# Optimization experiments

Hardware: AMD Instinct MI355X
Metric: run time of the kernel (lower is better)

## Reference

```python
import jax, jax.numpy as jnp
import numpy as np
import math

B, S, D, H = 16, 1024, 1024, 16
HD = D // H                      # 64 head dim
MLP_H = int(int(D * 4.0) * 2 / 3)  # 2730 SwiGLU hidden
EPS = 1e-6


def _rmsnorm(h, w):
    # fp32 RMSNorm over last dim
    v = jnp.mean(h * h, axis=-1, keepdims=True)
    return w * (h * jax.lax.rsqrt(v + EPS))


def _rope(x):
    # x: [B, H, S, HD]; standard rotary, half-split convention
    hd = x.shape[-1]
    pos = jnp.arange(x.shape[-2], dtype=jnp.float32)
    inv = 1.0 / (10000.0 ** (jnp.arange(0, hd, 2, dtype=jnp.float32) / hd))
    fr = pos[:, None] * inv[None, :]          # [S, HD/2]
    cos, sin = jnp.cos(fr), jnp.sin(fr)
    x1, x2 = jnp.split(x, 2, axis=-1)
    return jnp.concatenate([x1 * cos - x2 * sin, x1 * sin + x2 * cos], axis=-1)


def setup_inputs() -> dict:
    key = jax.random.key(0)
    ks = jax.random.split(key, 16)
    sc = 0.02
    return {
        "x": jax.random.normal(ks[0], (B, S, D), jnp.float32),
        "c": jax.random.normal(ks[1], (B, D), jnp.float32),
        "w_qkv": jax.random.normal(ks[2], (D, 3 * D), jnp.float32) * sc,
        "b_qkv": jnp.zeros((3 * D,), jnp.float32),
        "w_proj": jax.random.normal(ks[3], (D, D), jnp.float32) * sc,
        "b_proj": jnp.zeros((D,), jnp.float32),
        "w12": jax.random.normal(ks[4], (D, 2 * MLP_H), jnp.float32) * sc,
        "b12": jnp.zeros((2 * MLP_H,), jnp.float32),
        "w3": jax.random.normal(ks[5], (MLP_H, D), jnp.float32) * sc,
        "b3": jnp.zeros((D,), jnp.float32),
        "w_ada": jax.random.normal(ks[6], (D, 6 * D), jnp.float32) * sc,
        "b_ada": jnp.zeros((6 * D,), jnp.float32),
        "norm1_w": jnp.ones((D,), jnp.float32),
        "norm2_w": jnp.ones((D,), jnp.float32),
        "qn_w": jnp.ones((HD,), jnp.float32),
        "kn_w": jnp.ones((HD,), jnp.float32),
    }


def _forward(x, c, w_qkv, b_qkv, w_proj, b_proj, w12, b12, w3, b3,
             w_ada, b_ada, norm1_w, norm2_w, qn_w, kn_w):
    # adaLN modulation params
    ada = jax.nn.silu(c) @ w_ada + b_ada               # [B, 6D]
    sh_a, sc_a, g_a, sh_m, sc_m, g_m = jnp.split(ada, 6, axis=-1)

    def modulate(h, shift, scale):
        return h * (1.0 + scale[:, None, :]) + shift[:, None, :]

    # --- attention branch ---
    h = modulate(_rmsnorm(x, norm1_w), sh_a, sc_a)     # [B, S, D]
    qkv = (h @ w_qkv + b_qkv).reshape(B, S, 3, H, HD)
    qkv = jnp.transpose(qkv, (2, 0, 3, 1, 4))          # [3, B, H, S, HD]
    q, k, v = qkv[0], qkv[1], qkv[2]
    q = _rope(_rmsnorm(q, qn_w))
    k = _rope(_rmsnorm(k, kn_w))
    scores = jnp.einsum('bhqd,bhkd->bhqk', q, k) / math.sqrt(HD)
    attn = jax.nn.softmax(scores, axis=-1)
    o = jnp.einsum('bhqk,bhkd->bhqd', attn, v)         # [B, H, S, HD]
    o = jnp.transpose(o, (0, 2, 1, 3)).reshape(B, S, D)
    o = o @ w_proj + b_proj
    x = x + g_a[:, None, :] * o

    # --- SwiGLU MLP branch ---
    h = modulate(_rmsnorm(x, norm2_w), sh_m, sc_m)
    x12 = h @ w12 + b12
    x1, x2 = jnp.split(x12, 2, axis=-1)
    mlp = (jax.nn.silu(x1) * x2) @ w3 + b3
    return x + g_m[:, None, :] * mlp


def reference(x, c, w_qkv, b_qkv, w_proj, b_proj, w12, b12, w3, b3,
              w_ada, b_ada, norm1_w, norm2_w, qn_w, kn_w):
    return _forward(x, c, w_qkv, b_qkv, w_proj, b_proj, w12, b12, w3, b3,
                    w_ada, b_ada, norm1_w, norm2_w, qn_w, kn_w)
```

## Files before the change

### kernel.cpp

```cpp
#include <hip/hip_runtime.h>
#include <hip/hip_bf16.h>
#include <math.h>

namespace {

constexpr int Bb = 16;
constexpr int Ss = 1024;
constexpr int Dd = 1024;
constexpr int Hh = 16;
constexpr int HD = 64;
constexpr int MLPH = 2730;
constexpr int MLPH_PAD = 2752;
constexpr int ADA_LD = 6144;
constexpr int NR = Bb * Ss;

typedef __attribute__((ext_vector_type(8))) short bf16x8;
typedef __attribute__((ext_vector_type(4))) float f32x4;
typedef __hip_bfloat16 bf16;
typedef unsigned int u32;

__device__ __forceinline__ float bf2f(bf16 v){ return __bfloat162float(v); }
__device__ __forceinline__ bf16 f2bf(float v){ return __float2bfloat16(v); }
__device__ __forceinline__ short f2bfs(float v){ bf16 t = __float2bfloat16(v); return __builtin_bit_cast(short, t); }

__device__ __forceinline__ f32x4 mfma16(bf16x8 a, bf16x8 b, f32x4 c){
  return __builtin_amdgcn_mfma_f32_16x16x32_bf16(a, b, c, 0, 0, 0);
}

__device__ __forceinline__ void gload16(const void* g, void* l){
  __builtin_amdgcn_global_load_lds(
      (const __attribute__((address_space(1))) u32*)g,
      (__attribute__((address_space(3))) u32*)l, 16, 0, 0);
}

__device__ __forceinline__ bf16x8 dsr128(const short* p){
  f32x4 r;
  asm volatile("ds_read_b128 %0, %1" : "=v"(r) : "v"((u32)(size_t)p));
  return __builtin_bit_cast(bf16x8, r);
}


__global__ void k_silu(const float* __restrict__ c, float* __restrict__ out, int n){
  int i = blockIdx.x*256 + threadIdx.x;
  if(i < n){ float v = c[i]; out[i] = v / (1.f + __expf(-v)); }
}

__global__ __launch_bounds__(256) void k_ada(const float* __restrict__ sc,
    const float* __restrict__ w, const float* __restrict__ bias, float* __restrict__ ada){
  __shared__ float red[4][Bb][64];
  int tid = threadIdx.x;
  int jj = tid & 63, ks = tid >> 6;
  int j = blockIdx.x*64 + jj;
  float acc[Bb];
  #pragma unroll
  for(int b=0;b<Bb;++b) acc[b] = 0.f;
  for(int k=ks*256; k<ks*256+256; ++k){
    float wv = w[(size_t)k*ADA_LD + j];
    #pragma unroll
    for(int b=0;b<Bb;++b) acc[b] += sc[b*Dd + k] * wv;
  }
  #pragma unroll
  for(int b=0;b<Bb;++b) red[ks][b][jj] = acc[b];
  __syncthreads();
  #pragma unroll
  for(int rep=0;rep<4;++rep){
    int idx = rep*256 + tid;
    int b = idx >> 6, j2 = idx & 63;
    float s = red[0][b][j2]+red[1][b][j2]+red[2][b][j2]+red[3][b][j2];
    ada[(size_t)b*ADA_LD + blockIdx.x*64 + j2] = s + bias[blockIdx.x*64 + j2];
  }
}

__global__ void k_rope_tab(float2* __restrict__ tab){
  int i = blockIdx.x*256 + threadIdx.x;
  int s = i >> 5, f = i & 31;
  float inv = powf(10000.f, -((float)(2*f)) / 64.f);
  float fr = (float)s * inv;
  float sv, cv;
  sincosf(fr, &sv, &cv);
  tab[i] = make_float2(cv, sv);
}

__global__ void k_transpose(const float* __restrict__ in, bf16* __restrict__ out,
                            int R, int C, int Rpad){
  __shared__ short tile[32][33];
  int tx = threadIdx.x & 31, ty = threadIdx.x >> 5;
  int tr0 = blockIdx.x*32, tc0 = blockIdx.y*32;
  #pragma unroll
  for(int i=0;i<4;++i){
    int r = tr0 + ty + i*8, cc = tc0 + tx;
    short v = 0;
    if(r < R && cc < C) v = f2bfs(in[(size_t)r*C + cc]);
    tile[ty+i*8][tx] = v;
  }
  __syncthreads();
  #pragma unroll
  for(int i=0;i<4;++i){
    int oc = tc0 + ty + i*8;
    int orow = tr0 + tx;
    if(oc < C && orow < Rpad)
      out[(size_t)oc*Rpad + orow] = __builtin_bit_cast(bf16, tile[tx][ty+i*8]);
  }
}

__global__ __launch_bounds__(256) void k_norm_mod(const float* __restrict__ x,
    const float* __restrict__ w, const float* __restrict__ shift, const float* __restrict__ scale,
    bf16* __restrict__ out){
  int r = blockIdx.x;
  int b = r >> 10;
  int t = threadIdx.x;
  const float* xr = x + (size_t)r*Dd;
  float v[4]; float ss = 0.f;
  #pragma unroll
  for(int i=0;i<4;++i){
    float f = xr[t*4+i];
    v[i] = f; ss += f*f;
  }
  #pragma unroll
  for(int m=1;m<64;m<<=1) ss += __shfl_xor(ss, m);
  __shared__ float red[4];
  if((t & 63) == 0) red[t>>6] = ss;
  __syncthreads();
  float tot = red[0]+red[1]+red[2]+red[3];
  float rms = rsqrtf(tot * (1.f/Dd) + 1e-6f);
  #pragma unroll
  for(int i=0;i<4;++i){
    int ccol = t*4+i;
    float h = v[i]*rms*w[ccol];
    float scv = scale[(size_t)b*ADA_LD + ccol];
    float shv = shift[(size_t)b*ADA_LD + ccol];
    out[(size_t)r*Dd + ccol] = f2bf(h*(1.f+scv) + shv);
  }
}

__global__ __launch_bounds__(256) void k_qknorm(bf16* __restrict__ qkv,
    const float* __restrict__ qw, const float* __restrict__ kw,
    const float2* __restrict__ tab){
  int bs = blockIdx.x;
  int s = bs & (Ss-1);
  int tid = threadIdx.x;
  int wv = tid >> 6, lane = tid & 63;
  int isK = wv >> 1;
  int chunk = (wv & 1)*64 + lane;
  int c = chunk & 7;
  int h = chunk >> 3;
  int dih = c*8;
  bf16* p = qkv + (size_t)bs*3072 + isK*Dd + h*HD + dih;
  bf16x8 v = *(const bf16x8*)p;
  float x[8]; float ss = 0.f;
  #pragma unroll
  for(int i=0;i<8;++i){ x[i] = bf2f(__builtin_bit_cast(bf16,(short)v[i])); ss += x[i]*x[i]; }
  ss += __shfl_xor(ss,1); ss += __shfl_xor(ss,2); ss += __shfl_xor(ss,4);
  float rms = rsqrtf(ss*(1.f/HD) + 1e-6f);
  const float* wn = isK ? kw : qw;
  float xn[8];
  #pragma unroll
  for(int i=0;i<8;++i) xn[i] = x[i]*rms*wn[dih+i];
  u32 pk[4], pq[4];
  #pragma unroll
  for(int i=0;i<4;++i)
    pk[i] = (u32)(unsigned short)f2bfs(xn[2*i]) |
            ((u32)(unsigned short)f2bfs(xn[2*i+1]) << 16);
  #pragma unroll
  for(int i=0;i<4;++i) pq[i] = __shfl_xor((int)pk[i], 4);
  float px[8];
  #pragma unroll
  for(int i=0;i<4;++i){
    px[2*i]   = bf2f(__builtin_bit_cast(bf16,(short)(pq[i] & 0xffff)));
    px[2*i+1] = bf2f(__builtin_bit_cast(bf16,(short)(pq[i] >> 16)));
  }
  const float2* tb = tab + s*32 + (c & 3)*8;
  float qs = isK ? 1.f : 0.18033688f;
  bf16x8 o;
  #pragma unroll
  for(int i=0;i<8;++i){
    float2 cs = tb[i];
    float r = (c < 4) ? (xn[i]*cs.x - px[i]*cs.y) : (px[i]*cs.y + xn[i]*cs.x);
    o[i] = f2bfs(r*qs);
  }
  *(bf16x8*)p = o;
}

#define LDA8(M,KH) dsr128(&Ah[((M)*16 + l15)*64 + ((((KH)*4 + l4) ^ l7))*8])
#define PHASE8(M0, STAGE_STMT, GATE_STMT) do{ \
  bf16x8 a0k0 = LDA8(M0,0), a0k1 = LDA8(M0,1), a1k0 = LDA8(M0+1,0), a1k1 = LDA8(M0+1,1); \
  STAGE_STMT; \
  __builtin_amdgcn_s_barrier(); \
  asm volatile("s_waitcnt lgkmcnt(0)" ::: "memory"); \
  __builtin_amdgcn_sched_barrier(0); \
  __builtin_amdgcn_s_setprio(1); \
  acc[M0][0]=mfma16(a0k0,bfrag[0][0],acc[M0][0]); \
  acc[M0][1]=mfma16(a0k0,bfrag[1][0],acc[M0][1]); \
  acc[M0][2]=mfma16(a0k0,bfrag[2][0],acc[M0][2]); \
  acc[M0][3]=mfma16(a0k0,bfrag[3][0],acc[M0][3]); \
  acc[M0+1][0]=mfma16(a1k0,bfrag[0][0],acc[M0+1][0]); \
  acc[M0+1][1]=mfma16(a1k0,bfrag[1][0],acc[M0+1][1]); \
  acc[M0+1][2]=mfma16(a1k0,bfrag[2][0],acc[M0+1][2]); \
  acc[M0+1][3]=mfma16(a1k0,bfrag[3][0],acc[M0+1][3]); \
  acc[M0][0]=mfma16(a0k1,bfrag[0][1],acc[M0][0]); \
  acc[M0][1]=mfma16(a0k1,bfrag[1][1],acc[M0][1]); \
  acc[M0][2]=mfma16(a0k1,bfrag[2][1],acc[M0][2]); \
  acc[M0][3]=mfma16(a0k1,bfrag[3][1],acc[M0][3]); \
  acc[M0+1][0]=mfma16(a1k1,bfrag[0][1],acc[M0+1][0]); \
  acc[M0+1][1]=mfma16(a1k1,bfrag[1][1],acc[M0+1][1]); \
  acc[M0+1][2]=mfma16(a1k1,bfrag[2][1],acc[M0+1][2]); \
  acc[M0+1][3]=mfma16(a1k1,bfrag[3][1],acc[M0+1][3]); \
  __builtin_amdgcn_s_setprio(0); \
  GATE_STMT; \
  __builtin_amdgcn_s_barrier(); }while(0)

template<int MODE>
__global__ __launch_bounds__(512, 2) void k_gemm8(
    const bf16* __restrict__ A, int lda,
    const bf16* __restrict__ BT, int ldb,
    const float* __restrict__ bias1, int K,
    const float* __restrict__ res, const float* __restrict__ gate,
    void* __restrict__ outp, int ldo)
{
  alignas(16) __shared__ short AH[2][2][128*64];
  alignas(16) __shared__ short BH[2][2][128*64];

  const int tid = threadIdx.x;
  const int lane = tid & 63, wid = tid >> 6;
  const int wm = wid >> 2, wn = wid & 3;
  const int l15 = lane & 15, l4 = lane >> 4;
  const int l7 = l15 & 7;
  const int brow = blockIdx.x * 256;
  const int bcol = blockIdx.y * 256;

  const int sr0 = tid >> 3;
  const int sr1 = sr0 + 64;
  const int sc  = ((tid & 7) ^ (sr0 & 7)) * 8;

  const bf16* Abase = A  + (size_t)brow*lda;
  const bf16* Bbase = BT + (size_t)bcol*ldb;

  auto stageA = [&](int t, int h){
    int d = t & 1;
    const bf16* g = Abase + (size_t)(h*128)*lda + t*64;
    gload16(g + (size_t)sr0*lda + sc, &AH[d][h][tid*8]);
    gload16(g + (size_t)sr1*lda + sc, &AH[d][h][(tid+512)*8]);
  };
  auto stageB = [&](int t, int h){
    int d = t & 1;
    const bf16* g = Bbase + (size_t)(h*128)*ldb + t*64;
    gload16(g + (size_t)sr0*ldb + sc, &BH[d][h][tid*8]);
    gload16(g + (size_t)sr1*ldb + sc, &BH[d][h][(tid+512)*8]);
  };

  f32x4 acc[8][4];
  f32x4 zero4 = {0.f,0.f,0.f,0.f};
  #pragma unroll
  for(int m=0;m<8;++m)
    #pragma unroll
    for(int n=0;n<4;++n) acc[m][n] = zero4;

  const int NT = K >> 6;
  stageA(0,0); stageA(0,1); stageB(0,0); stageB(0,1);
  stageB(1,0); stageB(1,1);
  asm volatile("s_waitcnt vmcnt(4)" ::: "memory");
  __builtin_amdgcn_sched_barrier(0);
  __builtin_amdgcn_s_barrier();

  const int bhsel = wn >> 1, brB = (wn & 1)*64;
  bf16x8 bfrag[4][2];

  for(int t=0; t<NT; ++t){
    const int d = t & 1;
    const short* Ah = AH[d][wm];
    const short* Bh = BH[d][bhsel];
    #pragma unroll
    for(int n=0;n<4;++n){
      int r = brB + n*16 + l15;
      bfrag[n][0] = dsr128(&Bh[r*64 + ((l4     ^ l7))*8]);
      bfrag[n][1] = dsr128(&Bh[r*64 + (((4|l4) ^ l7))*8]);
    }
    PHASE8(0, if(t+1 < NT) stageA(t+1,0), );
    PHASE8(2, if(t+1 < NT) stageA(t+1,1), );
    PHASE8(4, if(t+2 < NT) stageB(t+2,0), );
    PHASE8(6, if(t+2 < NT) stageB(t+2,1),
           asm volatile("s_waitcnt vmcnt(4)" ::: "memory");
           __builtin_amdgcn_sched_barrier(0) );
  }

  #pragma unroll
  for(int m=0;m<8;++m)
    #pragma unroll
    for(int n=0;n<4;++n)
      #pragma unroll
      for(int j=0;j<4;++j){
        int r  = brow + wm*128 + m*16 + l4*4 + j;
        int cc = bcol + wn*64  + n*16 + l15;
        float v = acc[m][n][j] + bias1[cc];
        if constexpr (MODE==0){
          ((bf16*)outp)[(size_t)r*ldo + cc] = f2bf(v);
        } else {
          int b = r >> 10;
          ((float*)outp)[(size_t)r*ldo + cc] =
              res[(size_t)r*Dd + cc] + gate[(size_t)b*ADA_LD + cc]*v;
        }
      }
}

__global__ __launch_bounds__(256, 2) void k_gemm3(
    const bf16* __restrict__ A, int lda,
    const bf16* __restrict__ BT, long long b2off, int ldb,
    const float* __restrict__ bias1, const float* __restrict__ bias2,
    int K, bf16* __restrict__ outp, int ldo)
{
  alignas(16) __shared__ short As[2][128*32];
  alignas(16) __shared__ short Bs[2][64*32];
  alignas(16) __shared__ short Bs2[2][64*32];

  int tid = threadIdx.x;
  int lane = tid & 63, wid = tid >> 6;
  int wm = wid >> 1, wn = wid & 1;
  int l15 = lane & 15, l4 = lane >> 4;
  int brow = blockIdx.x * 128;
  int bcol = blockIdx.y * 64;

  int r0 = tid >> 2, s0 = tid & 3;
  int r1 = r0 + 64;
  int k80 = s0 ^ ((r0 >> 1) & 3);
  int k81 = s0 ^ ((r1 >> 1) & 3);

  const bf16* a0 = A  + (size_t)(brow+r0)*lda + k80*8;
  const bf16* a1 = A  + (size_t)(brow+r1)*lda + k81*8;
  const bf16* b0 = BT + (size_t)(bcol+r0)*ldb + k80*8;

  f32x4 zero4 = {0.f,0.f,0.f,0.f};
  f32x4 acc[4][2], acc2[4][2];
  #pragma unroll
  for(int m=0;m<4;++m)
    #pragma unroll
    for(int n=0;n<2;++n){ acc[m][n]=zero4; acc2[m][n]=zero4; }

  auto STAGE = [&](int kt, int buf){
    int ko = kt << 5;
    gload16(a0 + ko, &As[buf][tid*8]);
    gload16(a1 + ko, &As[buf][(tid+256)*8]);
    gload16(b0 + ko, &Bs[buf][tid*8]);
    gload16(b0 + b2off + ko, &Bs2[buf][tid*8]);
  };

  const int nk = K >> 5;
  STAGE(0, 0);
  __syncthreads();

  int cur = 0;
  for(int kt=0; kt<nk; ++kt){
    if(kt+1 < nk) STAGE(kt+1, cur^1);
    bf16x8 af[4], bfr[2], bfr2[2];
    #pragma unroll
    for(int m=0;m<4;++m){
      int rr = wm*64 + m*16 + l15;
      int sl = l4 ^ ((rr >> 1) & 3);
      af[m] = *(const bf16x8*)&As[cur][rr*32 + sl*8];
    }
    #pragma unroll
    for(int n=0;n<2;++n){
      int rr = wn*32 + n*16 + l15;
      int sl = l4 ^ ((rr >> 1) & 3);
      bfr[n]  = *(const bf16x8*)&Bs[cur][rr*32 + sl*8];
      bfr2[n] = *(const bf16x8*)&Bs2[cur][rr*32 + sl*8];
    }
    #pragma unroll
    for(int m=0;m<4;++m)
      #pragma unroll
      for(int n=0;n<2;++n){
        acc[m][n]  = mfma16(af[m], bfr[n],  acc[m][n]);
        acc2[m][n] = mfma16(af[m], bfr2[n], acc2[m][n]);
      }
    __syncthreads();
    cur ^= 1;
  }

  #pragma unroll
  for(int m=0;m<4;++m)
    #pragma unroll
    for(int n=0;n<2;++n)
      #pragma unroll
      for(int j=0;j<4;++j){
        int r  = brow + wm*64 + m*16 + l4*4 + j;
        int cc = bcol + wn*32 + n*16 + l15;
        float o = 0.f;
        if(cc < MLPH){
          float v1 = acc[m][n][j] + bias1[cc];
          float v2 = acc2[m][n][j] + bias2[cc];
          o = (v1/(1.f+__expf(-v1)))*v2;
        }
        outp[(size_t)r*ldo + cc] = f2bf(o);
      }
}

__global__ __launch_bounds__(256) void k_attn(const bf16* __restrict__ qkv, bf16* __restrict__ obuf){
  alignas(16) __shared__ short Ks[64*64];
  alignas(16) __shared__ short VTs[64*64];
  alignas(16) __shared__ short Ps[128*64];

  int flatb = blockIdx.x;
  int low3 = flatb & 7;
  int rest = flatb >> 3;
  int qb   = rest & 7;
  int bh   = ((rest >> 3) << 3) | low3;
  int b = bh >> 4, h = bh & 15;

  int tid = threadIdx.x;
  int lane = tid & 63, w = tid >> 6;
  int l15 = lane & 15, l4 = lane >> 4;

  const bf16* base = qkv + (size_t)b*Ss*3072 + h*HD;

  bf16x8 aq[2][2];
  #pragma unroll
  for(int hi=0;hi<2;++hi)
    #pragma unroll
    for(int hf=0;hf<2;++hf)
      aq[hi][hf] = *(const bf16x8*)(base +
          (size_t)(qb*128 + w*32 + hi*16 + l15)*3072 + hf*32 + l4*8);

  int r0 = tid >> 3, c0 = tid & 7;
  int khcol = (c0 ^ (r0 & 7)) * 8;
  bf16x8 kreg[2], vreg[2];
  #pragma unroll
  for(int ch=0; ch<2; ++ch){
    int rr = r0 + ch*32;
    kreg[ch] = *(const bf16x8*)(base + Dd   + (size_t)rr*3072 + khcol);
    vreg[ch] = *(const bf16x8*)(base + 2*Dd + (size_t)rr*3072 + c0*8);
  }

  f32x4 zero4 = {0.f,0.f,0.f,0.f};
  f32x4 acc_o[2][4];
  float mrow[2], lrow[2];
  #pragma unroll
  for(int hi=0;hi<2;++hi){
    mrow[hi] = -1e30f; lrow[hi] = 0.f;
    #pragma unroll
    for(int an=0;an<4;++an) acc_o[hi][an] = zero4;
  }

  const float THR = 11.54f;

  for(int kb=0; kb<Ss/64; ++kb){
    if(kb) __syncthreads();
    #pragma unroll
    for(int ch=0; ch<2; ++ch){
      *(bf16x8*)&Ks[(tid + ch*256)*8] = kreg[ch];
      int vr = r0 + ch*32;
      #pragma unroll
      for(int i=0;i<8;++i){
        int g = i ^ c0;
        VTs[(c0*8 + i)*64 + (vr ^ (g<<3))] = vreg[ch][i];
      }
    }
    if(kb+1 < Ss/64){
      #pragma unroll
      for(int ch=0; ch<2; ++ch){
        int rr = (kb+1)*64 + r0 + ch*32;
        kreg[ch] = *(const bf16x8*)(base + Dd   + (size_t)rr*3072 + khcol);
        vreg[ch] = *(const bf16x8*)(base + 2*Dd + (size_t)rr*3072 + c0*8);
      }
    }
    __syncthreads();

    bf16x8 kf[4][2];
    #pragma unroll
    for(int an=0;an<4;++an){
      int R = an*16 + l15;
      kf[an][0] = *(const bf16x8*)&Ks[R*64 + ((l4     ^ (R&7)))*8];
      kf[an][1] = *(const bf16x8*)&Ks[R*64 + (((4|l4) ^ (R&7)))*8];
    }
    f32x4 sacc[2][4];
    #pragma unroll
    for(int hi=0;hi<2;++hi)
      #pragma unroll
      for(int an=0;an<4;++an) sacc[hi][an] = zero4;
    __builtin_amdgcn_s_setprio(1);
    #pragma unroll
    for(int an=0;an<4;++an){
      sacc[0][an] = mfma16(kf[an][0], aq[0][0], sacc[0][an]);
      sacc[1][an] = mfma16(kf[an][0], aq[1][0], sacc[1][an]);
    }
    #pragma unroll
    for(int an=0;an<4;++an){
      sacc[0][an] = mfma16(kf[an][1], aq[0][1], sacc[0][an]);
      sacc[1][an] = mfma16(kf[an][1], aq[1][1], sacc[1][an]);
    }
    __builtin_amdgcn_s_setprio(0);

    #pragma unroll
    for(int hi=0; hi<2; ++hi){
      float mx = -1e30f;
      #pragma unroll
      for(int an=0;an<4;++an)
        #pragma unroll
        for(int j=0;j<4;++j) mx = fmaxf(mx, sacc[hi][an][j]);
      mx = fmaxf(mx, __shfl_xor(mx, 16));
      mx = fmaxf(mx, __shfl_xor(mx, 32));
      bool grow = mx > mrow[hi] + THR;
      if(__any(grow)){
        float mnew = fmaxf(mrow[hi], mx);
        float corr = exp2f(mrow[hi] - mnew);
        mrow[hi] = mnew;
        lrow[hi] *= corr;
        float cj[4];
        #pragma unroll
        for(int j=0;j<4;++j) cj[j] = __shfl(corr, l4*4 + j);
        #pragma unroll
        for(int an=0;an<4;++an)
          #pragma unroll
          for(int j=0;j<4;++j) acc_o[hi][an][j] *= cj[j];
      }
      float psum = 0.f;
      #pragma unroll
      for(int an=0;an<4;++an)
        #pragma unroll
        for(int j=0;j<4;++j){
          float pv = exp2f(sacc[hi][an][j] - mrow[hi]);
          sacc[hi][an][j] = pv; psum += pv;
        }
      psum += __shfl_xor(psum, 16);
      psum += __shfl_xor(psum, 32);
      lrow[hi] += psum;

      int prow = w*32 + hi*16 + l15;
      int pg = (l15 & 7) << 3;
      #pragma unroll
      for(int an=0;an<4;++an)
        #pragma unroll
        for(int j=0;j<4;++j)
          Ps[prow*64 + ((an*16 + l4*4 + j) ^ pg)] = f2bfs(sacc[hi][an][j]);
    }

    int pgme = (l15 & 7) << 3;
    bf16x8 pa[2][2];
    #pragma unroll
    for(int hi=0;hi<2;++hi){
      int prow = w*32 + hi*16 + l15;
      pa[hi][0] = *(const bf16x8*)&Ps[prow*64 + ((l4*8)      ^ pgme)];
      pa[hi][1] = *(const bf16x8*)&Ps[prow*64 + ((32 + l4*8) ^ pgme)];
    }
    bf16x8 vf[4][2];
    #pragma unroll
    for(int an2=0;an2<4;++an2){
      int dR = an2*16 + l15;
      int g = ((dR & 7) ^ ((dR >> 3) & 7)) << 3;
      vf[an2][0] = *(const bf16x8*)&VTs[dR*64 + ((l4*8)      ^ g)];
      vf[an2][1] = *(const bf16x8*)&VTs[dR*64 + ((32 + l4*8) ^ g)];
    }
    __builtin_amdgcn_s_setprio(1);
    #pragma unroll
    for(int an2=0;an2<4;++an2){
      acc_o[0][an2] = mfma16(pa[0][0], vf[an2][0], acc_o[0][an2]);
      acc_o[1][an2] = mfma16(pa[1][0], vf[an2][0], acc_o[1][an2]);
    }
    #pragma unroll
    for(int an2=0;an2<4;++an2){
      acc_o[0][an2] = mfma16(pa[0][1], vf[an2][1], acc_o[0][an2]);
      acc_o[1][an2] = mfma16(pa[1][1], vf[an2][1], acc_o[1][an2]);
    }
    __builtin_amdgcn_s_setprio(0);
  }

  #pragma unroll
  for(int hi=0;hi<2;++hi){
    float lr[4];
    #pragma unroll
    for(int j=0;j<4;++j) lr[j] = __shfl(lrow[hi], l4*4 + j);
    #pragma unroll
    for(int an2=0;an2<4;++an2)
      #pragma unroll
      for(int j=0;j<4;++j){
        int r = qb*128 + w*32 + hi*16 + l4*4 + j;
        float ov = acc_o[hi][an2][j] / lr[j];
        obuf[((size_t)b*Ss + r)*Dd + h*HD + an2*16 + l15] = f2bf(ov);
      }
  }
}

}

extern "C" void kernel_launch(void* const* d_in, const int* in_sizes, int n_in,
                              void* d_out, int out_size, void* d_ws, size_t ws_size,
                              hipStream_t stream){
  const float* x      = (const float*)d_in[0];
  const float* c      = (const float*)d_in[1];
  const float* w_qkv  = (const float*)d_in[2];
  const float* b_qkv  = (const float*)d_in[3];
  const float* w_proj = (const float*)d_in[4];
  const float* b_proj = (const float*)d_in[5];
  const float* w12    = (const float*)d_in[6];
  const float* b12    = (const float*)d_in[7];
  const float* w3     = (const float*)d_in[8];
  const float* b3     = (const float*)d_in[9];
  const float* w_ada  = (const float*)d_in[10];
  const float* b_ada  = (const float*)d_in[11];
  const float* n1w    = (const float*)d_in[12];
  const float* n2w    = (const float*)d_in[13];
  const float* qnw    = (const float*)d_in[14];
  const float* knw    = (const float*)d_in[15];
  float* out = (float*)d_out;
  (void)in_sizes; (void)n_in; (void)out_size;

  constexpr size_t WS_NEED = 227254272ull;
  if (ws_size < WS_NEED) return;

  char* ws = (char*)d_ws;
  float*  silu_c = (float*)(ws + 0);
  float*  ada    = (float*)(ws + 65536);
  float2* ropet  = (float2*)(ws + 458752);
  bf16*   wqkvT  = (bf16*)(ws + 720896);
  bf16*   wprojT = (bf16*)(ws + 7012352);
  bf16*   w12T   = (bf16*)(ws + 9109504);
  bf16*   w3T    = (bf16*)(ws + 20291584);
  bf16*   hbuf   = (bf16*)(ws + 25927680);
  bf16*   qkvb   = (bf16*)(ws + 59482112);
  float*  xmid   = (float*)(ws + 160145408);
  bf16*   obuf   = hbuf;
  bf16*   h2     = hbuf;
  bf16*   mlpmid = qkvb;

  k_silu<<<64,256,0,stream>>>(c, silu_c, Bb*Dd);
  k_rope_tab<<<128,256,0,stream>>>(ropet);
  k_ada<<<96,256,0,stream>>>(silu_c, w_ada, b_ada, ada);
  k_transpose<<<dim3(32,96),256,0,stream>>>(w_qkv, wqkvT, 1024, 3072, 1024);
  k_transpose<<<dim3(32,32),256,0,stream>>>(w_proj, wprojT, 1024, 1024, 1024);
  k_transpose<<<dim3(32,171),256,0,stream>>>(w12, w12T, 1024, 5460, 1024);
  k_transpose<<<dim3(86,32),256,0,stream>>>(w3, w3T, 2730, 1024, 2752);

  k_norm_mod<<<NR,256,0,stream>>>(x, n1w, ada + 0, ada + 1024, hbuf);
  k_gemm8<0><<<dim3(64,12),512,0,stream>>>(hbuf,1024, wqkvT,1024,
      b_qkv, 1024, nullptr,nullptr, qkvb,3072);
  k_qknorm<<<NR,256,0,stream>>>(qkvb, qnw, knw, ropet);
  k_attn<<<2048,256,0,stream>>>(qkvb, obuf);
  k_gemm8<1><<<dim3(64,4),512,0,stream>>>(obuf,1024, wprojT,1024,
      b_proj, 1024, x, ada + 2048, xmid,1024);

  k_norm_mod<<<NR,256,0,stream>>>(xmid, n2w, ada + 3072, ada + 4096, h2);
  k_gemm3<<<dim3(128,43),256,0,stream>>>(h2,1024, w12T,(long long)MLPH*1024,1024,
      b12, b12 + MLPH, 1024, mlpmid, MLPH_PAD);
  k_gemm8<1><<<dim3(64,4),512,0,stream>>>(mlpmid,MLPH_PAD, w3T,MLPH_PAD,
      b3, MLPH_PAD, xmid, ada + 5120, out,1024);
}
```

Before: 863.4 us.

## Triple-buffer LDS in the fused SwiGLU GEMM with explicit vmcnt waits

Replaces double buffering in k_gemm3 with a three-stage LDS ring, so tile kt+2 is prefetched while tile kt is computed. Waits use a partial vmcnt count, so only the tile about to be consumed must have landed. It adds scheduling barriers, setprio around the MFMA block and precomputed swizzled LDS offsets. The aim is to hide global-load latency behind MFMAs. LDS use rises by half, which could reduce occupancy at the launch bound of two blocks per CU, and correctness depends on the vmcnt(4) count matching the four loads per stage.

```diff
diff --git a/kernel.cpp b/kernel.cpp
--- a/kernel.cpp
+++ b/kernel.cpp
@@ -308,9 +308,9 @@
     const float* __restrict__ bias1, const float* __restrict__ bias2,
     int K, bf16* __restrict__ outp, int ldo)
 {
-  alignas(16) __shared__ short As[2][128*32];
-  alignas(16) __shared__ short Bs[2][64*32];
-  alignas(16) __shared__ short Bs2[2][64*32];
+  alignas(16) __shared__ short As[3][128*32];
+  alignas(16) __shared__ short Bs[3][64*32];
+  alignas(16) __shared__ short Bs2[3][64*32];
 
   int tid = threadIdx.x;
   int lane = tid & 63, wid = tid >> 6;
@@ -335,44 +335,64 @@
     #pragma unroll
     for(int n=0;n<2;++n){ acc[m][n]=zero4; acc2[m][n]=zero4; }
 
-  auto STAGE = [&](int kt, int buf){
+  auto STAGE = [&](int kt, int bi){
     int ko = kt << 5;
-    gload16(a0 + ko, &As[buf][tid*8]);
-    gload16(a1 + ko, &As[buf][(tid+256)*8]);
-    gload16(b0 + ko, &Bs[buf][tid*8]);
-    gload16(b0 + b2off + ko, &Bs2[buf][tid*8]);
+    gload16(a0 + ko, &As[bi][tid*8]);
+    gload16(a1 + ko, &As[bi][(tid+256)*8]);
+    gload16(b0 + ko, &Bs[bi][tid*8]);
+    gload16(b0 + b2off + ko, &Bs2[bi][tid*8]);
   };
 
   const int nk = K >> 5;
   STAGE(0, 0);
-  __syncthreads();
-
-  int cur = 0;
+  STAGE(1, 1);
+  asm volatile("s_waitcnt vmcnt(4)" ::: "memory");
+  __builtin_amdgcn_sched_barrier(0);
+  __builtin_amdgcn_s_barrier();
+
+  int arr[4], asl[4];
+  #pragma unroll
+  for(int m=0;m<4;++m){
+    arr[m] = wm*64 + m*16 + l15;
+    asl[m] = l4 ^ ((arr[m] >> 1) & 3);
+  }
+  int brr[2], bsl[2];
+  #pragma unroll
+  for(int n=0;n<2;++n){
+    brr[n] = wn*32 + n*16 + l15;
+    bsl[n] = l4 ^ ((brr[n] >> 1) & 3);
+  }
+
+  int bi = 0;
   for(int kt=0; kt<nk; ++kt){
-    if(kt+1 < nk) STAGE(kt+1, cur^1);
+    bool more = (kt+2) < nk;
+    int bn = bi+2; if(bn >= 3) bn -= 3;
+    if(more) STAGE(kt+2, bn);
+
     bf16x8 af[4], bfr[2], bfr2[2];
     #pragma unroll
+    for(int m=0;m<4;++m) af[m] = dsr128(&As[bi][arr[m]*32 + asl[m]*8]);
+    #pragma unroll
+    for(int n=0;n<2;++n){
+      bfr[n]  = dsr128(&Bs[bi][brr[n]*32 + bsl[n]*8]);
+      bfr2[n] = dsr128(&Bs2[bi][brr[n]*32 + bsl[n]*8]);
+    }
+    asm volatile("s_waitcnt lgkmcnt(0)" ::: "memory");
+    __builtin_amdgcn_sched_barrier(0);
+    __builtin_amdgcn_s_setprio(1);
+    #pragma unroll
     for(int m=0;m<4;++m){
-      int rr = wm*64 + m*16 + l15;
-      int sl = l4 ^ ((rr >> 1) & 3);
-      af[m] = *(const bf16x8*)&As[cur][rr*32 + sl*8];
-    }
-    #pragma unroll
-    for(int n=0;n<2;++n){
-      int rr = wn*32 + n*16 + l15;
-      int sl = l4 ^ ((rr >> 1) & 3);
-      bfr[n]  = *(const bf16x8*)&Bs[cur][rr*32 + sl*8];
-      bfr2[n] = *(const bf16x8*)&Bs2[cur][rr*32 + sl*8];
-    }
-    #pragma unroll
-    for(int m=0;m<4;++m)
-      #pragma unroll
-      for(int n=0;n<2;++n){
-        acc[m][n]  = mfma16(af[m], bfr[n],  acc[m][n]);
-        acc2[m][n] = mfma16(af[m], bfr2[n], acc2[m][n]);
-      }
-    __syncthreads();
-    cur ^= 1;
+      acc[m][0]  = mfma16(af[m], bfr[0],  acc[m][0]);
+      acc2[m][0] = mfma16(af[m], bfr2[0], acc2[m][0]);
+      acc[m][1]  = mfma16(af[m], bfr[1],  acc[m][1]);
+      acc2[m][1] = mfma16(af[m], bfr2[1], acc2[m][1]);
+    }
+    __builtin_amdgcn_s_setprio(0);
+    if(more){ asm volatile("s_waitcnt vmcnt(4)" ::: "memory"); }
+    else    { asm volatile("s_waitcnt vmcnt(0)" ::: "memory"); }
+    __builtin_amdgcn_sched_barrier(0);
+    __builtin_amdgcn_s_barrier();
+    ++bi; if(bi >= 3) bi = 0;
   }
 
   #pragma unroll
```

After: 863.2 us (median of 2 runs). Within noise of the previous version (-0.0%).
